# Optimization experiments

Measured on AMD Instinct MI355X. Metric: run time of the kernel, lower is better.

The kernel has to match this reference:

```python
import jax, jax.numpy as jnp
import numpy as np

B, S, D, H = 2, 2048, 1024, 16
HD = D // H  # head_dim = 64
NEG_INF = -jnp.inf


def _rope_tables(seq_len, head_dim, theta=10000.0):
    inv = 1.0 / (theta ** (np.arange(0, head_dim, 2, dtype=np.float32) / head_dim))
    t = np.arange(seq_len, dtype=np.float32)
    ang = np.outer(t, inv)  # [S, HD/2]
    return jnp.asarray(np.cos(ang)), jnp.asarray(np.sin(ang))


def _apply_rope(x, cos, sin):
    # x: [B, S, H, HD]; pairs (even, odd) rotated by complex freqs, matching
    # torch.view_as_complex(reshape(..., -1, 2)) * freqs_cis.
    x2 = x.reshape(*x.shape[:-1], HD // 2, 2)
    x0, x1 = x2[..., 0], x2[..., 1]
    c = cos[None, :, None, :]
    s = sin[None, :, None, :]
    o0 = x0 * c - x1 * s
    o1 = x0 * s + x1 * c
    return jnp.stack([o0, o1], axis=-1).reshape(x.shape)


def setup_inputs() -> dict:
    key = jax.random.key(0)
    ks = jax.random.split(key, 10)
    sc = 1.0 / np.sqrt(D)
    return {
        "x": jax.random.normal(ks[0], (B, S, D), dtype=jnp.float32),
        "effective_len": jax.random.randint(ks[1], (B,), 0, 1024, dtype=jnp.int32),
        "Wq": jax.random.normal(ks[2], (D, D), dtype=jnp.float32) * sc,
        "bq": jnp.zeros((D,), dtype=jnp.float32),
        "Wk": jax.random.normal(ks[3], (D, D), dtype=jnp.float32) * sc,
        "bk": jnp.zeros((D,), dtype=jnp.float32),
        "Wv": jax.random.normal(ks[4], (D, D), dtype=jnp.float32) * sc,
        "bv": jnp.zeros((D,), dtype=jnp.float32),
        "Wo": jax.random.normal(ks[5], (D, D), dtype=jnp.float32) * sc,
        "bo": jnp.zeros((D,), dtype=jnp.float32),
    }


def reference(x, effective_len, Wq, bq, Wk, bk, Wv, bv, Wo, bo):
    cos, sin = _rope_tables(S, HD)
    q = (x @ Wq.T + bq).reshape(B, S, H, HD)
    k = (x @ Wk.T + bk).reshape(B, S, H, HD)
    v = (x @ Wv.T + bv).reshape(B, S, H, HD)
    q = _apply_rope(q, cos, sin)
    k = _apply_rope(k, cos, sin)
    # [B, H, S, S]
    scores = jnp.einsum("bqhd,bkhd->bhqk", q, k) / np.sqrt(HD)
    row = jnp.arange(S)[:, None]
    col = jnp.arange(S)[None, :]
    causal = jnp.where(col > row, NEG_INF, 0.0)  # [S, S]
    scores = scores + causal[None, None, :, :]
    # faithful replication of original: masks the LAST effective_len key columns
    pad = jnp.where(col[None, 0, :] >= (S - effective_len)[:, None], NEG_INF, 0.0)  # [B, S]
    scores = scores + pad[:, None, None, :]
    probs = jax.nn.softmax(scores.astype(jnp.float32), axis=-1).astype(x.dtype)
    out = jnp.einsum("bhqk,bkhd->bqhd", probs, v).reshape(B, S, D)
    return out @ Wo.T + bo  # dropout in eval mode = identity
```

## Files before the change

kernel.cpp:

```cpp
#include <hip/hip_runtime.h>

#define SB   2048
#define DD   1024
#define NH   16
#define HDIM 64
#define NB   2

typedef float f4 __attribute__((ext_vector_type(4)));
typedef __bf16 bf16x8 __attribute__((ext_vector_type(8)));
typedef unsigned short u16;
typedef unsigned int u32;
typedef unsigned long long u64;
typedef u16 u16x8 __attribute__((ext_vector_type(8)));
typedef u16 u16x4 __attribute__((ext_vector_type(4)));

#define QSCALE 0.1803368801111f

__device__ __forceinline__ u16 f2bf(float f) {
  unsigned u = __float_as_uint(f);
  u += 0x7FFFu + ((u >> 16) & 1u);
  return (u16)(u >> 16);
}

typedef __attribute__((address_space(3))) unsigned int lds_uint;
typedef __attribute__((address_space(1))) const unsigned int glb_uint;
__device__ __forceinline__ void gl_lds16(const void* g, void* l) {
  __builtin_amdgcn_global_load_lds((glb_uint*)g, (lds_uint*)l, 16, 0, 0);
}

__device__ __forceinline__ void cvt8(const float* __restrict__ src,
                                     u16* __restrict__ dst, size_t i) {
  f4 a = *(const f4*)(src + 8 * i);
  f4 b = *(const f4*)(src + 8 * i + 4);
  u16x8 o;
  o[0] = f2bf(a[0]); o[1] = f2bf(a[1]); o[2] = f2bf(a[2]); o[3] = f2bf(a[3]);
  o[4] = f2bf(b[0]); o[5] = f2bf(b[1]); o[6] = f2bf(b[2]); o[7] = f2bf(b[3]);
  *(u16x8*)(dst + 8 * i) = o;
}

__global__ __launch_bounds__(256) void prep_kernel(
    const float* __restrict__ x, const float* __restrict__ Wq,
    const float* __restrict__ Wk, const float* __restrict__ Wv,
    u16* __restrict__ xb, u16* __restrict__ Wb3,
    float* __restrict__ cosT, float* __restrict__ sinT) {
  int bid = blockIdx.x, t = threadIdx.x;
  if (bid < 2048) {
    cvt8(x, xb, (size_t)bid * 256 + t);
  } else if (bid < 2560) {
    cvt8(Wq, Wb3, (size_t)(bid - 2048) * 256 + t);
  } else if (bid < 3072) {
    cvt8(Wk, Wb3 + (1u << 20), (size_t)(bid - 2560) * 256 + t);
  } else if (bid < 3584) {
    cvt8(Wv, Wb3 + (2u << 20), (size_t)(bid - 3072) * 256 + t);
  } else {
    int idx = (bid - 3584) * 256 + t;
    int tt = idx & 31, s = idx >> 5;
    float inv = powf(10000.0f, -2.0f * (float)tt / 64.0f);
    float ang = (float)s * inv;
    cosT[idx] = cosf(ang);
    sinT[idx] = sinf(ang);
  }
}

__global__ __launch_bounds__(256) void cvt_bf16_kernel(const float* __restrict__ src,
                                                       u16* __restrict__ dst) {
  cvt8(src, dst, (size_t)blockIdx.x * 256 + threadIdx.x);
}

__global__ __launch_bounds__(256) void gemm_qkv_fused_kernel(
    const u16* __restrict__ A, const u16* __restrict__ W3,
    const float* __restrict__ bq, const float* __restrict__ bk,
    const float* __restrict__ bv,
    u16* __restrict__ Qw, u16* __restrict__ Kw, u16* __restrict__ Vt,
    const float* __restrict__ cosT, const float* __restrict__ sinT) {
  const int K = DD;
  __shared__ u16 As[128 * 64];
  __shared__ u16 Bs[128 * 64];
  const int t = threadIdx.x;
  const int wave = t >> 6, lane = t & 63;
  const int m0 = blockIdx.x * 128, n0 = blockIdx.y * 128;
  const int mw = (wave >> 1) * 64, nw = (wave & 1) * 64;
  const int quad = lane >> 4, l15 = lane & 15;
  const int srow = lane >> 3, sgran = lane & 7;
  const u16* Ab = A + (size_t)m0 * K;
  const u16* Bb = W3 + (size_t)n0 * K;
  f4 acc[4][4];
#pragma unroll
  for (int i = 0; i < 4; i++)
#pragma unroll
    for (int j = 0; j < 4; j++) acc[i][j] = (f4)0.f;

  for (int kt = 0; kt < K; kt += 64) {
#pragma unroll
    for (int is = 0; is < 4; is++) {
      int r = wave * 32 + is * 8 + srow;
      int lg = sgran ^ (r & 7);
      gl_lds16(Ab + (size_t)r * K + kt + lg * 8, &As[(wave * 32 + is * 8) * 64]);
      gl_lds16(Bb + (size_t)r * K + kt + lg * 8, &Bs[(wave * 32 + is * 8) * 64]);
    }
    __syncthreads();
#pragma unroll
    for (int kh = 0; kh < 2; kh++) {
      bf16x8 af[4], bfr[4];
#pragma unroll
      for (int i = 0; i < 4; i++) {
        int R = mw + 16 * i + l15;
        af[i] = *(const bf16x8*)&As[R * 64 + ((kh * 4 + quad) ^ (R & 7)) * 8];
        int Rb = nw + 16 * i + l15;
        bfr[i] = *(const bf16x8*)&Bs[Rb * 64 + ((kh * 4 + quad) ^ (Rb & 7)) * 8];
      }
#pragma unroll
      for (int i = 0; i < 4; i++)
#pragma unroll
        for (int j = 0; j < 4; j++)
          acc[i][j] = __builtin_amdgcn_mfma_f32_16x16x32_bf16(af[i], bfr[j],
                                                              acc[i][j], 0, 0, 0);
    }
    __syncthreads();
  }

#pragma unroll
  for (int j = 0; j < 4; j++) {
    int colg3 = n0 + nw + 16 * j + l15;
    int which = colg3 >> 10;
    int c = colg3 & 1023;
    int h = c >> 6, dh = c & 63, tt2 = dh >> 1;
    float bval = (which == 0 ? bq : which == 1 ? bk : bv)[c];
    if (which == 2) {
#pragma unroll
      for (int i = 0; i < 4; i++) {
        int mg0 = m0 + mw + 16 * i + quad * 4;
        int b = mg0 >> 11, sr0 = mg0 & (SB - 1);
        u16x4 pk4;
#pragma unroll
        for (int r = 0; r < 4; r++) pk4[r] = f2bf(acc[i][j][r] + bval);
        *(u16x4*)(Vt + ((size_t)(b * NH + h) * HDIM + dh) * SB + sr0) = pk4;
      }
    } else {
      u16* dst = which ? Kw : Qw;
      float scale = which ? 1.0f : QSCALE;
#pragma unroll
      for (int i = 0; i < 4; i++)
#pragma unroll
        for (int r = 0; r < 4; r++) {
          int mg = m0 + mw + 16 * i + quad * 4 + r;
          int b = mg >> 11, sr = mg & (SB - 1);
          float v = acc[i][j][r] + bval;
          float vp = __shfl_xor(v, 1);
          float cc = cosT[sr * 32 + tt2], ss = sinT[sr * 32 + tt2];
          v = ((lane & 1) == 0) ? (v * cc - vp * ss) : (vp * ss + v * cc);
          dst[(((size_t)(b * NH + h)) * SB + sr) * HDIM + dh] = f2bf(v * scale);
        }
    }
  }
}

__global__ __launch_bounds__(256) void gemm_out_kernel(
    const u16* __restrict__ A, const u16* __restrict__ W,
    const float* __restrict__ bias, float* __restrict__ outp) {
  const int K = DD;
  __shared__ u16 As[128 * 64];
  __shared__ u16 Bs[64 * 64];
  const int t = threadIdx.x;
  const int wave = t >> 6, lane = t & 63;
  const int m0 = blockIdx.x * 128, n0 = blockIdx.y * 64;
  const int mw = (wave >> 1) * 64, nw = (wave & 1) * 32;
  const int quad = lane >> 4, l15 = lane & 15;
  const int srow = lane >> 3, sgran = lane & 7;
  const u16* Ab = A + (size_t)m0 * K;
  const u16* Bb = W + (size_t)n0 * K;
  f4 acc[4][2];
#pragma unroll
  for (int i = 0; i < 4; i++)
#pragma unroll
    for (int j = 0; j < 2; j++) acc[i][j] = (f4)0.f;

  for (int kt = 0; kt < K; kt += 64) {
#pragma unroll
    for (int is = 0; is < 4; is++) {
      int r = wave * 32 + is * 8 + srow;
      int lg = sgran ^ (r & 7);
      gl_lds16(Ab + (size_t)r * K + kt + lg * 8, &As[(wave * 32 + is * 8) * 64]);
    }
#pragma unroll
    for (int is = 0; is < 2; is++) {
      int r = wave * 16 + is * 8 + srow;
      int lg = sgran ^ (r & 7);
      gl_lds16(Bb + (size_t)r * K + kt + lg * 8, &Bs[(wave * 16 + is * 8) * 64]);
    }
    __syncthreads();
#pragma unroll
    for (int kh = 0; kh < 2; kh++) {
      bf16x8 af[4], bfr[2];
#pragma unroll
      for (int i = 0; i < 4; i++) {
        int R = mw + 16 * i + l15;
        af[i] = *(const bf16x8*)&As[R * 64 + ((kh * 4 + quad) ^ (R & 7)) * 8];
      }
#pragma unroll
      for (int j = 0; j < 2; j++) {
        int R = nw + 16 * j + l15;
        bfr[j] = *(const bf16x8*)&Bs[R * 64 + ((kh * 4 + quad) ^ (R & 7)) * 8];
      }
#pragma unroll
      for (int i = 0; i < 4; i++)
#pragma unroll
        for (int j = 0; j < 2; j++)
          acc[i][j] = __builtin_amdgcn_mfma_f32_16x16x32_bf16(af[i], bfr[j],
                                                              acc[i][j], 0, 0, 0);
    }
    __syncthreads();
  }
#pragma unroll
  for (int i = 0; i < 4; i++)
#pragma unroll
    for (int j = 0; j < 2; j++) {
      int colg = n0 + nw + 16 * j + l15;
#pragma unroll
      for (int r = 0; r < 4; r++) {
        int mg = m0 + mw + 16 * i + quad * 4 + r;
        outp[(size_t)mg * DD + colg] = acc[i][j][r] + bias[colg];
      }
    }
}

__global__ __launch_bounds__(512) void attn_mfma_kernel(
    const u16* __restrict__ Qw, const u16* __restrict__ Kw,
    const u16* __restrict__ Vt, u16* __restrict__ Ow,
    const int* __restrict__ eff) {
  __shared__ u16 KL[2][8 * 64 * 8];
  __shared__ u16 VL[2][8 * 64 * 8];
  const int w = threadIdx.x >> 6, lane = threadIdx.x & 63;
  const int l15 = lane & 15, q4 = lane >> 4;
  const int qp = blockIdx.x;
  const int wg = w >> 2, wl = w & 3;
  const int QT = wg ? (SB / 128 - 1 - qp) : qp;
  const int h = blockIdx.y, b = blockIdx.z;
  const int limit = SB - eff[b];
  const size_t bh = ((size_t)b * NH + h) * (SB * HDIM);

  const int rowbase = QT * 128 + wl * 32;

  bf16x8 qf[2][2];
  {
    const u16* qp0 = Qw + bh + (size_t)(rowbase + l15) * HDIM + q4 * 8;
    qf[0][0] = *(const bf16x8*)qp0;
    qf[0][1] = *(const bf16x8*)(qp0 + 32);
    const u16* qp1 = qp0 + 16 * HDIM;
    qf[1][0] = *(const bf16x8*)qp1;
    qf[1][1] = *(const bf16x8*)(qp1 + 32);
  }

  f4 acc[2][4];
#pragma unroll
  for (int s = 0; s < 2; s++)
#pragma unroll
    for (int dt = 0; dt < 4; dt++) acc[s][dt] = (f4)0.f;
  float l_run[2] = {0.f, 0.f};

  const int kendB = min((SB / 128 - 1 - qp) * 128 + 127, limit - 1);
  const int ntiles = (kendB >> 6) + 1;
  const int wkend = min(rowbase + 31, limit - 1);

#define STAGE_TILE(TILE, BUF)                                                   \
  {                                                                             \
    const int colb_ = (TILE) * 64;                                              \
    _Pragma("unroll") for (int f = 0; f < 2; f++) {                             \
      int fr = w * 2 + f;                                                       \
      if (fr < 8) {                                                             \
        int mt = fr >> 1, j = fr & 1;                                           \
        gl_lds16(Kw + bh + (size_t)(colb_ + mt * 16 + l15) * HDIM + q4 * 8 + j * 32, \
                 &KL[BUF][fr * 512]);                                           \
      } else {                                                                  \
        int fv = fr - 8, dt = fv >> 1, j = fv & 1;                              \
        gl_lds16(Vt + bh + (size_t)(dt * 16 + l15) * SB + colb_ + q4 * 8 + j * 32, \
                 &VL[BUF][fv * 512]);                                           \
      }                                                                         \
    }                                                                           \
  }

  STAGE_TILE(0, 0)
  __syncthreads();

  for (int kt = 0; kt < ntiles; kt++) {
    const int cur = kt & 1;
    const int colb = kt * 64;
    if (kt + 1 < ntiles) STAGE_TILE(kt + 1, cur ^ 1)

    if (colb <= wkend) {
      f4 sa[2][4];
#pragma unroll
      for (int mt = 0; mt < 4; mt++) {
        bf16x8 k0 = *(const bf16x8*)&KL[cur][(mt * 2 + 0) * 512 + lane * 8];
        bf16x8 k1 = *(const bf16x8*)&KL[cur][(mt * 2 + 1) * 512 + lane * 8];
        f4 s0 = (f4)0.f, s1 = (f4)0.f;
        s0 = __builtin_amdgcn_mfma_f32_16x16x32_bf16(k0, qf[0][0], s0, 0, 0, 0);
        s0 = __builtin_amdgcn_mfma_f32_16x16x32_bf16(k1, qf[0][1], s0, 0, 0, 0);
        s1 = __builtin_amdgcn_mfma_f32_16x16x32_bf16(k0, qf[1][0], s1, 0, 0, 0);
        s1 = __builtin_amdgcn_mfma_f32_16x16x32_bf16(k1, qf[1][1], s1, 0, 0, 0);
        sa[0][mt] = s0;
        sa[1][mt] = s1;
      }

      u32 pk[2][4][2];
#pragma unroll
      for (int s = 0; s < 2; s++) {
        const int rb = rowbase + 16 * s;
        const int rg = rb + l15;
        const bool needmask = (colb + 63 > rb) || (colb + 63 >= limit);
        if (needmask) {
#pragma unroll
          for (int mt = 0; mt < 4; mt++)
#pragma unroll
            for (int r = 0; r < 4; r++) {
              int col = colb + mt * 16 + q4 * 4 + r;
              if (col > rg || col >= limit) sa[s][mt][r] = -3.0e38f;
            }
        }
        float lsum = 0.f;
#pragma unroll
        for (int mt = 0; mt < 4; mt++) {
          float p0 = exp2f(sa[s][mt][0]);
          float p1 = exp2f(sa[s][mt][1]);
          float p2 = exp2f(sa[s][mt][2]);
          float p3 = exp2f(sa[s][mt][3]);
          lsum += (p0 + p1) + (p2 + p3);
          pk[s][mt][0] = (__float_as_uint(p1) & 0xFFFF0000u) | (__float_as_uint(p0) >> 16);
          pk[s][mt][1] = (__float_as_uint(p3) & 0xFFFF0000u) | (__float_as_uint(p2) >> 16);
        }
        l_run[s] += lsum;
      }

      const int srcA = ((q4 & 1) << 5) + l15;
      const int hi = q4 >> 1;
#pragma unroll
      for (int s = 0; s < 2; s++) {
        union { u32 wds[4]; bf16x8 v; } ub0, ub1;
#pragma unroll
        for (int d = 0; d < 4; d++) {
          int src = srcA + ((d >> 1) << 4);
          u32 t0 = (u32)__shfl((int)pk[s][0][d & 1], src);
          u32 t1 = (u32)__shfl((int)pk[s][1][d & 1], src);
          ub0.wds[d] = hi ? t1 : t0;
          u32 t2 = (u32)__shfl((int)pk[s][2][d & 1], src);
          u32 t3 = (u32)__shfl((int)pk[s][3][d & 1], src);
          ub1.wds[d] = hi ? t3 : t2;
        }
#pragma unroll
        for (int dt = 0; dt < 4; dt++) {
          bf16x8 v0 = *(const bf16x8*)&VL[cur][(dt * 2 + 0) * 512 + lane * 8];
          bf16x8 v1 = *(const bf16x8*)&VL[cur][(dt * 2 + 1) * 512 + lane * 8];
          acc[s][dt] = __builtin_amdgcn_mfma_f32_16x16x32_bf16(v0, ub0.v, acc[s][dt], 0, 0, 0);
          acc[s][dt] = __builtin_amdgcn_mfma_f32_16x16x32_bf16(v1, ub1.v, acc[s][dt], 0, 0, 0);
        }
      }
    }
    __syncthreads();
  }

#pragma unroll
  for (int s = 0; s < 2; s++) {
    float lt = l_run[s];
    lt += __shfl_xor(lt, 16);
    lt += __shfl_xor(lt, 32);
    const float linv = 1.0f / lt;
    const int rg = rowbase + 16 * s + l15;
    const size_t obase = (((size_t)b * SB + rg) * NH + h) * HDIM + q4 * 4;
#pragma unroll
    for (int dt = 0; dt < 4; dt++) {
      u16x4 o;
      o[0] = f2bf(acc[s][dt][0] * linv);
      o[1] = f2bf(acc[s][dt][1] * linv);
      o[2] = f2bf(acc[s][dt][2] * linv);
      o[3] = f2bf(acc[s][dt][3] * linv);
      *(u16x4*)(Ow + obase + dt * 16) = o;
    }
  }
}

extern "C" void kernel_launch(void* const* d_in, const int* in_sizes, int n_in,
                              void* d_out, int out_size, void* d_ws, size_t ws_size,
                              hipStream_t stream) {
  (void)in_sizes; (void)n_in; (void)out_size; (void)ws_size;
  const float* x  = (const float*)d_in[0];
  const int*   eff = (const int*)d_in[1];
  const float* Wq = (const float*)d_in[2];
  const float* bq = (const float*)d_in[3];
  const float* Wk = (const float*)d_in[4];
  const float* bk = (const float*)d_in[5];
  const float* Wv = (const float*)d_in[6];
  const float* bv = (const float*)d_in[7];
  const float* Wo = (const float*)d_in[8];
  const float* bo = (const float*)d_in[9];
  float* out = (float*)d_out;

  char* ws = (char*)d_ws;
  u16* Qw = (u16*)(ws);
  u16* Kw = (u16*)(ws + (8u << 20));
  u16* Vt = (u16*)(ws + (16u << 20));
  u16* Ow = (u16*)(ws + (24u << 20));
  u16* xb = (u16*)(ws + (24u << 20));
  u16* Wb3 = (u16*)(ws + (32u << 20));
  float* cosT = (float*)(ws + (38u << 20));
  float* sinT = (float*)(ws + (38u << 20) + (256u << 10));

  hipLaunchKernelGGL(prep_kernel, dim3(3840), dim3(256), 0, stream,
                     x, Wq, Wk, Wv, xb, Wb3, cosT, sinT);

  hipLaunchKernelGGL(gemm_qkv_fused_kernel, dim3(32, 24), dim3(256), 0, stream,
                     xb, Wb3, bq, bk, bv, Qw, Kw, Vt, cosT, sinT);

  hipLaunchKernelGGL(cvt_bf16_kernel, dim3(512), dim3(256), 0, stream, Wo, Wb3);

  hipLaunchKernelGGL(attn_mfma_kernel, dim3(SB / 256, NH, NB), dim3(512), 0, stream,
                     Qw, Kw, Vt, Ow, eff);

  hipLaunchKernelGGL(gemm_out_kernel, dim3(32, 16), dim3(256), 0, stream, Ow, Wb3, bo, out);
}
```

Before: 203.0 us.

## Stage QK epilogue through LDS for vectorized RoPE stores and fold Wo conversion into prep

```diff
diff --git a/kernel.cpp b/kernel.cpp
--- a/kernel.cpp
+++ b/kernel.cpp
@@ -41,8 +41,9 @@
 __global__ __launch_bounds__(256) void prep_kernel(
     const float* __restrict__ x, const float* __restrict__ Wq,
     const float* __restrict__ Wk, const float* __restrict__ Wv,
-    u16* __restrict__ xb, u16* __restrict__ Wb3,
-    float* __restrict__ cosT, float* __restrict__ sinT) {
+    const float* __restrict__ Wo,
+    u16* __restrict__ xb, u16* __restrict__ Wb3, u16* __restrict__ WoB,
+    float* __restrict__ cosT, float* __restrict__ sinT, int nwo) {
   int bid = blockIdx.x, t = threadIdx.x;
   if (bid < 2048) {
     cvt8(x, xb, (size_t)bid * 256 + t);
@@ -52,8 +53,10 @@
     cvt8(Wk, Wb3 + (1u << 20), (size_t)(bid - 2560) * 256 + t);
   } else if (bid < 3584) {
     cvt8(Wv, Wb3 + (2u << 20), (size_t)(bid - 3072) * 256 + t);
+  } else if (bid < 3584 + nwo) {
+    cvt8(Wo, WoB, (size_t)(bid - 3584) * 256 + t);
   } else {
-    int idx = (bid - 3584) * 256 + t;
+    int idx = (bid - 3584 - nwo) * 256 + t;
     int tt = idx & 31, s = idx >> 5;
     float inv = powf(10000.0f, -2.0f * (float)tt / 64.0f);
     float ang = (float)s * inv;
@@ -74,8 +77,9 @@
     u16* __restrict__ Qw, u16* __restrict__ Kw, u16* __restrict__ Vt,
     const float* __restrict__ cosT, const float* __restrict__ sinT) {
   const int K = DD;
-  __shared__ u16 As[128 * 64];
-  __shared__ u16 Bs[128 * 64];
+  __shared__ char smem[32768];
+  u16* As = (u16*)smem;
+  u16* Bs = (u16*)(smem + 16384);
   const int t = threadIdx.x;
   const int wave = t >> 6, lane = t & 63;
   const int m0 = blockIdx.x * 128, n0 = blockIdx.y * 128;
@@ -119,14 +123,15 @@
     __syncthreads();
   }
 
-#pragma unroll
-  for (int j = 0; j < 4; j++) {
-    int colg3 = n0 + nw + 16 * j + l15;
-    int which = colg3 >> 10;
-    int c = colg3 & 1023;
-    int h = c >> 6, dh = c & 63, tt2 = dh >> 1;
-    float bval = (which == 0 ? bq : which == 1 ? bk : bv)[c];
-    if (which == 2) {
+  const int which = n0 >> 10;
+  const int hh = ((n0 & 1023) + nw) >> 6;
+  const int cb = (n0 + nw) & 1023;
+
+  if (which == 2) {
+#pragma unroll
+    for (int j = 0; j < 4; j++) {
+      const int dh = 16 * j + l15;
+      const float bval = bv[cb + 16 * j + l15];
 #pragma unroll
       for (int i = 0; i < 4; i++) {
         int mg0 = m0 + mw + 16 * i + quad * 4;
@@ -134,23 +139,62 @@
         u16x4 pk4;
 #pragma unroll
         for (int r = 0; r < 4; r++) pk4[r] = f2bf(acc[i][j][r] + bval);
-        *(u16x4*)(Vt + ((size_t)(b * NH + h) * HDIM + dh) * SB + sr0) = pk4;
-      }
-    } else {
-      u16* dst = which ? Kw : Qw;
-      float scale = which ? 1.0f : QSCALE;
-#pragma unroll
-      for (int i = 0; i < 4; i++)
-#pragma unroll
-        for (int r = 0; r < 4; r++) {
-          int mg = m0 + mw + 16 * i + quad * 4 + r;
-          int b = mg >> 11, sr = mg & (SB - 1);
-          float v = acc[i][j][r] + bval;
-          float vp = __shfl_xor(v, 1);
-          float cc = cosT[sr * 32 + tt2], ss = sinT[sr * 32 + tt2];
-          v = ((lane & 1) == 0) ? (v * cc - vp * ss) : (vp * ss + v * cc);
-          dst[(((size_t)(b * NH + h)) * SB + sr) * HDIM + dh] = f2bf(v * scale);
+        *(u16x4*)(Vt + ((size_t)(b * NH + hh) * HDIM + dh) * SB + sr0) = pk4;
+      }
+    }
+  } else {
+    u16* dst = which ? Kw : Qw;
+    const float* barr = which ? bk : bq;
+    const float scale = which ? 1.0f : QSCALE;
+    float bvj[4];
+#pragma unroll
+    for (int j = 0; j < 4; j++) bvj[j] = barr[cb + 16 * j + l15];
+    float* sl = (float*)(smem + wave * 8192);
+    const int kk = lane >> 1, hf = lane & 1;
+#pragma unroll
+    for (int half = 0; half < 2; half++) {
+#pragma unroll
+      for (int il = 0; il < 2; il++) {
+#pragma unroll
+        for (int j = 0; j < 4; j++) {
+          const int q = 4 * j + (l15 >> 2);
+          const int w = l15 & 3;
+#pragma unroll
+          for (int r = 0; r < 4; r++) {
+            const int row = il * 16 + quad * 4 + r;
+            sl[(row << 6) + (((q + row) & 15) << 2) + w] =
+                (acc[half * 2 + il][j][r] + bvj[j]) * scale;
+          }
         }
+      }
+      asm volatile("s_waitcnt lgkmcnt(0)" ::: "memory");
+      const int m = m0 + mw + half * 32 + kk;
+      const int b = m >> 11, sr = m & (SB - 1);
+      f4 cv[4], sv[4];
+      {
+        const f4* ct = (const f4*)(cosT + sr * 32 + hf * 16);
+        const f4* st2 = (const f4*)(sinT + sr * 32 + hf * 16);
+#pragma unroll
+        for (int p = 0; p < 4; p++) { cv[p] = ct[p]; sv[p] = st2[p]; }
+      }
+      u16x8 ov[4];
+#pragma unroll
+      for (int c8 = 0; c8 < 8; c8++) {
+        const int qc = hf * 8 + c8;
+        f4 v = *(const f4*)(sl + (kk << 6) + (((qc + kk) & 15) << 2));
+        const float c0 = cv[c8 >> 1][(c8 & 1) * 2];
+        const float s0 = sv[c8 >> 1][(c8 & 1) * 2];
+        const float c1 = cv[c8 >> 1][(c8 & 1) * 2 + 1];
+        const float s1 = sv[c8 >> 1][(c8 & 1) * 2 + 1];
+        ov[c8 >> 1][(c8 & 1) * 4 + 0] = f2bf(v[0] * c0 - v[1] * s0);
+        ov[c8 >> 1][(c8 & 1) * 4 + 1] = f2bf(v[0] * s0 + v[1] * c0);
+        ov[c8 >> 1][(c8 & 1) * 4 + 2] = f2bf(v[2] * c1 - v[3] * s1);
+        ov[c8 >> 1][(c8 & 1) * 4 + 3] = f2bf(v[2] * s1 + v[3] * c1);
+      }
+      u16* op = dst + (((size_t)(b * NH + hh)) * SB + sr) * HDIM + hf * 32;
+#pragma unroll
+      for (int q8 = 0; q8 < 4; q8++) *(u16x8*)(op + q8 * 8) = ov[q8];
+      if (half == 0) asm volatile("s_waitcnt lgkmcnt(0)" ::: "memory");
     }
   }
 }
@@ -381,7 +425,7 @@
 extern "C" void kernel_launch(void* const* d_in, const int* in_sizes, int n_in,
                               void* d_out, int out_size, void* d_ws, size_t ws_size,
                               hipStream_t stream) {
-  (void)in_sizes; (void)n_in; (void)out_size; (void)ws_size;
+  (void)in_sizes; (void)n_in; (void)out_size;
   const float* x  = (const float*)d_in[0];
   const int*   eff = (const int*)d_in[1];
   const float* Wq = (const float*)d_in[2];
@@ -404,16 +448,21 @@
   float* cosT = (float*)(ws + (38u << 20));
   float* sinT = (float*)(ws + (38u << 20) + (256u << 10));
 
-  hipLaunchKernelGGL(prep_kernel, dim3(3840), dim3(256), 0, stream,
-                     x, Wq, Wk, Wv, xb, Wb3, cosT, sinT);
+  size_t wob_off = (38u << 20) + (512u << 10);
+  int nwo = (ws_size >= wob_off + (2u << 20)) ? 512 : 0;
+  u16* WoB = nwo ? (u16*)(ws + wob_off) : Wb3;
+
+  hipLaunchKernelGGL(prep_kernel, dim3(3840 + nwo), dim3(256), 0, stream,
+                     x, Wq, Wk, Wv, Wo, xb, Wb3, WoB, cosT, sinT, nwo);
 
   hipLaunchKernelGGL(gemm_qkv_fused_kernel, dim3(32, 24), dim3(256), 0, stream,
                      xb, Wb3, bq, bk, bv, Qw, Kw, Vt, cosT, sinT);
 
-  hipLaunchKernelGGL(cvt_bf16_kernel, dim3(512), dim3(256), 0, stream, Wo, Wb3);
+  if (!nwo)
+    hipLaunchKernelGGL(cvt_bf16_kernel, dim3(512), dim3(256), 0, stream, Wo, WoB);
 
   hipLaunchKernelGGL(attn_mfma_kernel, dim3(SB / 256, NH, NB), dim3(512), 0, stream,
                      Qw, Kw, Vt, Ow, eff);
 
-  hipLaunchKernelGGL(gemm_out_kernel, dim3(32, 16), dim3(256), 0, stream, Ow, Wb3, bo, out);
-}
+  hipLaunchKernelGGL(gemm_out_kernel, dim3(32, 16), dim3(256), 0, stream, Ow, WoB, bo, out);
+}
```

After: 219.4 us. 1.08x slower.
